# Kernel tuning notes

Measured on AMD Instinct MI355X. Metric: run time of the kernel, lower is better.

## Reference

```python
import jax, jax.numpy as jnp
import numpy as np

N_EMBD = 1024  # C in forward; scale is C**-0.5 (full embed dim, per source)


def setup_inputs() -> dict:
    key = jax.random.key(0)
    k1, k2, k3, k4 = jax.random.split(key, 4)
    B, T, C, H = 4, 4096, N_EMBD, 64
    x = jax.random.normal(k1, (B, T, C), dtype=jnp.float32)
    # weights stored as [in, out] = [n_embd, head_size]
    Wq = jax.random.normal(k2, (C, H), dtype=jnp.float32) * (C ** -0.5)
    Wk = jax.random.normal(k3, (C, H), dtype=jnp.float32) * (C ** -0.5)
    Wv = jax.random.normal(k4, (C, H), dtype=jnp.float32) * (C ** -0.5)
    return {"x": x, "Wq": Wq, "Wk": Wk, "Wv": Wv}


def reference(x, Wq, Wk, Wv):
    # x: [B, T, C]; projections to head_size H
    C = x.shape[-1]
    q = jnp.einsum('btc,ch->bth', x, Wq)  # [B,T,H]
    k = jnp.einsum('btc,ch->bth', x, Wk)  # [B,T,H]
    v = jnp.einsum('btc,ch->bth', x, Wv)  # [B,T,H]
    # scores scaled by C**-0.5 (full embed dim, matching original module)
    wei = jnp.einsum('bth,bsh->bts', q, k) * (C ** -0.5)  # [B,T,T]
    wei = jax.nn.softmax(wei, axis=-1)  # dropout p=0 -> identity
    out = jnp.einsum('bts,bsh->bth', wei, v)  # [B,T,H]
    return out
```

## Files before the change

kernel.cpp:

```cpp
#include <hip/hip_runtime.h>
#include <hip/hip_bf16.h>


#define BB 4
#define TT 4096
#define CC 1024
#define HH 64

typedef __attribute__((ext_vector_type(8))) short bf16x8;
typedef __attribute__((ext_vector_type(4))) float f32x4;

#if __has_builtin(__builtin_amdgcn_exp2f)
#define EXP2(x) __builtin_amdgcn_exp2f(x)
#else
#define EXP2(x) exp2f(x)
#endif

__device__ __forceinline__ short f2bf(float f) {
  union { float f; unsigned u; } v; v.f = f;
  unsigned r = v.u + 0x7fffu + ((v.u >> 16) & 1u);
  return (short)(r >> 16);
}

__device__ __forceinline__ unsigned pk2bf(float lo, float hi) {
  __hip_bfloat162 p = __float22bfloat162_rn(make_float2(lo, hi));
  return *reinterpret_cast<unsigned*>(&p);
}

__global__ void wtf_kernel(const float* __restrict__ Wq, const float* __restrict__ Wk,
                           const float* __restrict__ Wv, short* __restrict__ WtF) {
  int idx = blockIdx.x * 256 + threadIdx.x;
  int lane = idx & 63, ks = (idx >> 6) & 31, nf = idx >> 11;
  int l15 = lane & 15, lg = lane >> 4;
  int n = nf * 16 + l15;
  const float* W = (n < HH) ? Wq : ((n < 2 * HH) ? Wk : Wv);
  float sc = (n < HH) ? (0.03125f * 1.44269504f) : 1.0f;
  int k0 = ks * 32 + lg * 8, h = n & (HH - 1);
  bf16x8 r;
#pragma unroll
  for (int j = 0; j < 8; ++j) r[j] = f2bf(W[(k0 + j) * HH + h] * sc);
  *(bf16x8*)(WtF + (size_t)idx * 8) = r;
}

__launch_bounds__(256, 4)
__global__ void proj_kernel(const float* __restrict__ x, const short* __restrict__ WtF,
                            short* __restrict__ qo, short* __restrict__ kFo,
                            short* __restrict__ vFo) {
  __shared__ __align__(16) short xs[16 * 1024];
  int t = threadIdx.x;
  int row0 = blockIdx.x * 16;

  {
    int r = t >> 4, kc = t & 15;
    const float4* xr4 = (const float4*)(x + (size_t)(row0 + r) * CC) + kc * 2;
#pragma unroll
    for (int i = 0; i < 8; ++i) {
      float4 a = xr4[i * 32], b2 = xr4[i * 32 + 1];
      uint4 w;
      w.x = pk2bf(a.x, a.y);   w.y = pk2bf(a.z, a.w);
      w.z = pk2bf(b2.x, b2.y); w.w = pk2bf(b2.z, b2.w);
      int c = kc + i * 16;
      int S = (c * 256 + r * 16) ^ ((c & 7) << 4);
      *(uint4*)((char*)xs + S) = w;
    }
  }
  __syncthreads();

  int wave = t >> 6, lane = t & 63;
  int l15 = lane & 15, lg = lane >> 4;
  int nf0 = wave * 3;
  const short* wp = WtF + ((size_t)nf0 * 32 * 64 + (size_t)lane) * 8;
  const char* xsb = (const char*)xs;

  f32x4 acc[3];
#pragma unroll
  for (int j = 0; j < 3; ++j) acc[j] = (f32x4){0.f, 0.f, 0.f, 0.f};

  bf16x8 wA[3], wB[3];
#pragma unroll
  for (int j = 0; j < 3; ++j) wA[j] = *(const bf16x8*)(wp + (size_t)j * 32 * 512);

#pragma unroll
  for (int ks = 0; ks < 32; ks += 2) {
#pragma unroll
    for (int j = 0; j < 3; ++j)
      wB[j] = *(const bf16x8*)(wp + ((size_t)j * 32 + ks + 1) * 512);
    bf16x8 a0 = *(const bf16x8*)(xsb + ks * 1024 +
                   ((lane * 16) ^ ((((ks * 4) + lg) & 7) << 4)));
#pragma unroll
    for (int j = 0; j < 3; ++j)
      acc[j] = __builtin_amdgcn_mfma_f32_16x16x32_bf16(a0, wA[j], acc[j], 0, 0, 0);
    if (ks + 2 < 32) {
#pragma unroll
      for (int j = 0; j < 3; ++j)
        wA[j] = *(const bf16x8*)(wp + ((size_t)j * 32 + ks + 2) * 512);
    }
    bf16x8 a1 = *(const bf16x8*)(xsb + (ks + 1) * 1024 +
                   ((lane * 16) ^ (((((ks + 1) * 4) + lg) & 7) << 4)));
#pragma unroll
    for (int j = 0; j < 3; ++j)
      acc[j] = __builtin_amdgcn_mfma_f32_16x16x32_bf16(a1, wB[j], acc[j], 0, 0, 0);
  }

  int b  = row0 >> 12;
  int kt = (row0 & 4095) >> 6;
  int cf = (row0 >> 4) & 3;
  short* ksl = xs;
  short* vsl = xs + 1152;

  __syncthreads();

#pragma unroll
  for (int j = 0; j < 3; ++j) {
    int nf = nf0 + j;
    int h = (nf & 3) * 16 + l15;
    if (nf < 4) {
#pragma unroll
      for (int reg = 0; reg < 4; ++reg)
        qo[(size_t)(row0 + lg * 4 + reg) * HH + h] = f2bf(acc[j][reg]);
    } else if (nf < 8) {
#pragma unroll
      for (int reg = 0; reg < 4; ++reg)
        ksl[(lg * 4 + reg) * 72 + h] = f2bf(acc[j][reg]);
    } else {
      uint2 w2;
      w2.x = pk2bf(acc[j][0], acc[j][1]);
      w2.y = pk2bf(acc[j][2], acc[j][3]);
      *(uint2*)(vsl + h * 24 + lg * 4) = w2;
    }
  }
  __syncthreads();

  size_t tileoff = ((size_t)b * 64 + kt) * 4096;
  if (t < 128) {
    int ks2 = t >> 6, ln = t & 63;
    int l15o = ln & 15, lgo = ln >> 4;
    bf16x8 r = *(const bf16x8*)(ksl + l15o * 72 + ks2 * 32 + lgo * 8);
    *(bf16x8*)(kFo + tileoff + (size_t)(cf * 2 + ks2) * 512 + ln * 8) = r;
  } else if (t < 256) {
    int t2 = t - 128;
    int hf = t2 >> 5, lgl = (t2 >> 4) & 1, l15o = t2 & 15;
    bf16x8 r = *(const bf16x8*)(vsl + (hf * 16 + l15o) * 24 + lgl * 8);
    int lnout = (2 * (cf & 1) + lgl) * 16 + l15o;
    *(bf16x8*)(vFo + tileoff + (size_t)(hf * 2 + (cf >> 1)) * 512 + lnout * 8) = r;
  }
}

__launch_bounds__(512, 4)
__global__ void attnW_kernel(const short* __restrict__ q, const short* __restrict__ kF,
                             const short* __restrict__ vF, float* __restrict__ out) {
  __shared__ __align__(16) short ps[8][2560];
  __shared__ __align__(16) float macc[32][68];
  __shared__ float lL[32];
  int wave = threadIdx.x >> 6, lane = threadIdx.x & 63;
  int l15 = lane & 15, lg = lane >> 4;
  int low3 = blockIdx.x & 7;
  int b  = low3 >> 1;
  int qt = ((blockIdx.x >> 3) << 1) | (low3 & 1);
  int brow0 = qt * 32;

  const short* qb = q + ((size_t)b * TT + brow0 + l15) * HH;
  bf16x8 qa[2][2];
#pragma unroll
  for (int g = 0; g < 2; ++g) {
    qa[g][0] = *(const bf16x8*)(qb + g * 16 * HH + lg * 8);
    qa[g][1] = *(const bf16x8*)(qb + g * 16 * HH + 32 + lg * 8);
  }

  bf16x8 ones;
#pragma unroll
  for (int j = 0; j < 8; ++j) ones[j] = (short)0x3F80;

  const short* kfb = kF + (size_t)b * 262144 + (size_t)lane * 8;
  const short* vfb = vF + (size_t)b * 262144 + (size_t)lane * 8;

  f32x4 acc[2][4], accl[2];
#pragma unroll
  for (int g = 0; g < 2; ++g) {
#pragma unroll
    for (int i = 0; i < 4; ++i) acc[g][i] = (f32x4){0.f, 0.f, 0.f, 0.f};
    accl[g] = (f32x4){0.f, 0.f, 0.f, 0.f};
  }

  char* psw = (char*)&ps[wave][0];
  int xorv = (l15 >> 3) << 4;
  int pwbase = l15 * 80;
  int pr = l15 * 80 + ((lg << 4) ^ xorv);

  for (int t = wave * 16; t < wave * 16 + 16; ++t) {
    const short* kp = kfb + (size_t)t * 2048;
    const short* vp = vfb + (size_t)(t >> 1) * 4096 + (size_t)(t & 1) * 512;
    bf16x8 kf[4], vf[4];
#pragma unroll
    for (int ld = 0; ld < 4; ++ld) kf[ld] = *(const bf16x8*)(kp + ld * 512);
#pragma unroll
    for (int hf = 0; hf < 4; ++hf) vf[hf] = *(const bf16x8*)(vp + hf * 1024);
#pragma unroll
    for (int g = 0; g < 2; ++g)
#pragma unroll
      for (int cf = 0; cf < 2; ++cf) {
        f32x4 t4 = (f32x4){0.f, 0.f, 0.f, 0.f};
        t4 = __builtin_amdgcn_mfma_f32_16x16x32_bf16(kf[cf * 2], qa[g][0], t4, 0, 0, 0);
        t4 = __builtin_amdgcn_mfma_f32_16x16x32_bf16(kf[cf * 2 + 1], qa[g][1], t4, 0, 0, 0);
        float p0 = EXP2(t4[0]), p1 = EXP2(t4[1]);
        float p2 = EXP2(t4[2]), p3 = EXP2(t4[3]);
        unsigned w01 = pk2bf(p0, p1);
        unsigned w23 = pk2bf(p2, p3);
        int cb = (cf << 5) + (lg << 3);
        *(unsigned*)(psw + g * 1280 + pwbase + ((cb) ^ xorv)) = w01;
        *(unsigned*)(psw + g * 1280 + pwbase + ((cb + 4) ^ xorv)) = w23;
      }
    bf16x8 pa0 = *(const bf16x8*)(psw + pr);
    bf16x8 pa1 = *(const bf16x8*)(psw + 1280 + pr);
    __builtin_amdgcn_s_setprio(1);
#pragma unroll
    for (int hf = 0; hf < 4; ++hf) {
      acc[0][hf] = __builtin_amdgcn_mfma_f32_16x16x32_bf16(pa0, vf[hf], acc[0][hf], 0, 0, 0);
      acc[1][hf] = __builtin_amdgcn_mfma_f32_16x16x32_bf16(pa1, vf[hf], acc[1][hf], 0, 0, 0);
    }
    accl[0] = __builtin_amdgcn_mfma_f32_16x16x32_bf16(pa0, ones, accl[0], 0, 0, 0);
    accl[1] = __builtin_amdgcn_mfma_f32_16x16x32_bf16(pa1, ones, accl[1], 0, 0, 0);
    __builtin_amdgcn_s_setprio(0);
  }

#pragma unroll
  for (int ph = 0; ph < 8; ++ph) {
    if (wave == ph) {
#pragma unroll
      for (int g = 0; g < 2; ++g)
#pragma unroll
        for (int reg = 0; reg < 4; ++reg) {
          int row = g * 16 + lg * 4 + reg;
          if (ph == 0) {
#pragma unroll
            for (int hf = 0; hf < 4; ++hf)
              macc[row][hf * 16 + l15] = acc[g][hf][reg];
            if (l15 == 0) lL[row] = accl[g][reg];
          } else {
#pragma unroll
            for (int hf = 0; hf < 4; ++hf)
              macc[row][hf * 16 + l15] += acc[g][hf][reg];
            if (l15 == 0) lL[row] += accl[g][reg];
          }
        }
    }
    __syncthreads();
  }

  {
    int tt = threadIdx.x;
    int r = tt >> 4, c0 = (tt & 15) * 4;
    float linv = 1.0f / lL[r];
    float4 o;
    o.x = macc[r][c0 + 0] * linv; o.y = macc[r][c0 + 1] * linv;
    o.z = macc[r][c0 + 2] * linv; o.w = macc[r][c0 + 3] * linv;
    *(float4*)(out + ((size_t)b * TT + brow0 + r) * HH + c0) = o;
  }
}

extern "C" void kernel_launch(void* const* d_in, const int* in_sizes, int n_in,
                              void* d_out, int out_size, void* d_ws, size_t ws_size,
                              hipStream_t stream) {
  const float* x  = (const float*)d_in[0];
  const float* Wq = (const float*)d_in[1];
  const float* Wk = (const float*)d_in[2];
  const float* Wv = (const float*)d_in[3];
  float* out = (float*)d_out;

  char* ws = (char*)d_ws;
  short* WtF = (short*)ws;
  short* q   = (short*)(ws + 0x080000);
  short* kF  = (short*)(ws + 0x280000);
  short* vF  = (short*)(ws + 0x480000);

  hipLaunchKernelGGL(wtf_kernel,   dim3(96),   dim3(256), 0, stream, Wq, Wk, Wv, WtF);
  hipLaunchKernelGGL(proj_kernel,  dim3(1024), dim3(256), 0, stream, x, WtF, q, kF, vF);
  hipLaunchKernelGGL(attnW_kernel, dim3(512),  dim3(512), 0, stream, q, kF, vF, out);
}
```

Baseline: 64.14 us.

## Pre-convert x to bf16 fragment layout and load it via global_load_lds

Adds a separate kernel that converts x from fp32 to bf16 and writes it in MFMA fragment order into workspace. The projection kernel then copies its tile straight into LDS with global_load_lds instead of converting in registers with swizzled stores, and reads fragments without swizzle math. The aim is to make the projection's load path cheaper and asynchronous. The cost is an extra launch plus a write and re-read of 32 MB of bf16 data, which may cost more than it saves since the projection is memory bound on x.

```diff
diff --git a/kernel.cpp b/kernel.cpp
--- a/kernel.cpp
+++ b/kernel.cpp
@@ -27,6 +27,14 @@
   return *reinterpret_cast<unsigned*>(&p);
 }
 
+__device__ __forceinline__ void gload16(const short* g, short* l) {
+  __builtin_amdgcn_global_load_lds(
+      (const __attribute__((address_space(1))) void*)g,
+      (__attribute__((address_space(3))) void*)l, 16, 0, 0);
+}
+
+#define WAITVM0() asm volatile("s_waitcnt vmcnt(0)" ::: "memory")
+
 __global__ void wtf_kernel(const float* __restrict__ Wq, const float* __restrict__ Wk,
                            const float* __restrict__ Wv, short* __restrict__ WtF) {
   int idx = blockIdx.x * 256 + threadIdx.x;
@@ -42,39 +50,45 @@
   *(bf16x8*)(WtF + (size_t)idx * 8) = r;
 }
 
+__global__ void xc_kernel(const float* __restrict__ x, short* __restrict__ xF) {
+  int idx = blockIdx.x * 256 + threadIdx.x;
+  int lane = idx & 63, ks = (idx >> 6) & 31, rt = idx >> 11;
+  int l15 = lane & 15, lg = lane >> 4;
+  const float4* src = (const float4*)(x + (size_t)(rt * 16 + l15) * CC + ks * 32 + lg * 8);
+  float4 a = src[0], b = src[1];
+  uint4 w;
+  w.x = pk2bf(a.x, a.y);  w.y = pk2bf(a.z, a.w);
+  w.z = pk2bf(b.x, b.y);  w.w = pk2bf(b.z, b.w);
+  *(uint4*)(xF + (size_t)idx * 8) = w;
+}
+
 __launch_bounds__(256, 4)
-__global__ void proj_kernel(const float* __restrict__ x, const short* __restrict__ WtF,
-                            short* __restrict__ qo, short* __restrict__ kFo,
-                            short* __restrict__ vFo) {
-  __shared__ __align__(16) short xs[16 * 1024];
+__global__ void projG_kernel(const short* __restrict__ xF, const short* __restrict__ WtF,
+                             short* __restrict__ qo, short* __restrict__ kFo,
+                             short* __restrict__ vFo) {
+  __shared__ __align__(16) short xs[16384];
   int t = threadIdx.x;
   int row0 = blockIdx.x * 16;
+  int wave = t >> 6, lane = t & 63;
+  int l15 = lane & 15, lg = lane >> 4;
 
   {
-    int r = t >> 4, kc = t & 15;
-    const float4* xr4 = (const float4*)(x + (size_t)(row0 + r) * CC) + kc * 2;
-#pragma unroll
-    for (int i = 0; i < 8; ++i) {
-      float4 a = xr4[i * 32], b2 = xr4[i * 32 + 1];
-      uint4 w;
-      w.x = pk2bf(a.x, a.y);   w.y = pk2bf(a.z, a.w);
-      w.z = pk2bf(b2.x, b2.y); w.w = pk2bf(b2.z, b2.w);
-      int c = kc + i * 16;
-      int S = (c * 256 + r * 16) ^ ((c & 7) << 4);
-      *(uint4*)((char*)xs + S) = w;
-    }
-  }
-  __syncthreads();
-
-  int wave = t >> 6, lane = t & 63;
-  int l15 = lane & 15, lg = lane >> 4;
+    const short* gsrc = xF + (size_t)blockIdx.x * 16384 + ((size_t)wave * 512 + lane) * 8;
+    short* ldst = xs + (size_t)wave * 4096;
+#pragma unroll
+    for (int k2 = 0; k2 < 8; ++k2)
+      gload16(gsrc + k2 * 512, ldst + k2 * 512);
+  }
+
   int nf0 = wave * 3;
   const short* wp = WtF + ((size_t)nf0 * 32 * 64 + (size_t)lane) * 8;
-  const char* xsb = (const char*)xs;
 
   f32x4 acc[3];
 #pragma unroll
   for (int j = 0; j < 3; ++j) acc[j] = (f32x4){0.f, 0.f, 0.f, 0.f};
+
+  WAITVM0();
+  __syncthreads();
 
   bf16x8 wA[3], wB[3];
 #pragma unroll
@@ -85,8 +99,7 @@
 #pragma unroll
     for (int j = 0; j < 3; ++j)
       wB[j] = *(const bf16x8*)(wp + ((size_t)j * 32 + ks + 1) * 512);
-    bf16x8 a0 = *(const bf16x8*)(xsb + ks * 1024 +
-                   ((lane * 16) ^ ((((ks * 4) + lg) & 7) << 4)));
+    bf16x8 a0 = *(const bf16x8*)(xs + ks * 512 + lane * 8);
 #pragma unroll
     for (int j = 0; j < 3; ++j)
       acc[j] = __builtin_amdgcn_mfma_f32_16x16x32_bf16(a0, wA[j], acc[j], 0, 0, 0);
@@ -95,8 +108,7 @@
       for (int j = 0; j < 3; ++j)
         wA[j] = *(const bf16x8*)(wp + ((size_t)j * 32 + ks + 2) * 512);
     }
-    bf16x8 a1 = *(const bf16x8*)(xsb + (ks + 1) * 1024 +
-                   ((lane * 16) ^ (((((ks + 1) * 4) + lg) & 7) << 4)));
+    bf16x8 a1 = *(const bf16x8*)(xs + (ks + 1) * 512 + lane * 8);
 #pragma unroll
     for (int j = 0; j < 3; ++j)
       acc[j] = __builtin_amdgcn_mfma_f32_16x16x32_bf16(a1, wB[j], acc[j], 0, 0, 0);
@@ -272,8 +284,10 @@
   short* q   = (short*)(ws + 0x080000);
   short* kF  = (short*)(ws + 0x280000);
   short* vF  = (short*)(ws + 0x480000);
+  short* xF  = (short*)(ws + 0x680000);
 
   hipLaunchKernelGGL(wtf_kernel,   dim3(96),   dim3(256), 0, stream, Wq, Wk, Wv, WtF);
-  hipLaunchKernelGGL(proj_kernel,  dim3(1024), dim3(256), 0, stream, x, WtF, q, kF, vF);
+  hipLaunchKernelGGL(xc_kernel,    dim3(8192), dim3(256), 0, stream, x, xF);
+  hipLaunchKernelGGL(projG_kernel, dim3(1024), dim3(256), 0, stream, xF, WtF, q, kF, vF);
   hipLaunchKernelGGL(attnW_kernel, dim3(512),  dim3(512), 0, stream, q, kF, vF, out);
 }
```

Measured after the change: 73.82 us. 1.15x slower.

## Stream projection weights into LDS with an async multi-stage global_load_lds ring

Applied to the files above, without the earlier changes.

The projection kernel no longer double-buffers weight fragments in registers. It issues asynchronous global_load_lds transfers into a 4-slot per-wave LDS ring, prefetching three k-steps ahead and gating each step with explicit vmcnt waits. The goal is to hide weight-fetch latency behind the MFMA loop and free registers. The cost is an extra 48KB of LDS per block and launch bounds dropped from 4 to 2, so occupancy for the x-streaming phase falls.

```diff
diff --git a/kernel.cpp b/kernel.cpp
--- a/kernel.cpp
+++ b/kernel.cpp
@@ -26,6 +26,14 @@
   __hip_bfloat162 p = __float22bfloat162_rn(make_float2(lo, hi));
   return *reinterpret_cast<unsigned*>(&p);
 }
+
+__device__ __forceinline__ void gload16(const short* g, short* l) {
+  __builtin_amdgcn_global_load_lds(
+      (const __attribute__((address_space(1))) void*)g,
+      (__attribute__((address_space(3))) void*)l, 16, 0, 0);
+}
+
+#define WAITVM(N) asm volatile("s_waitcnt vmcnt(" #N ")" ::: "memory")
 
 __global__ void wtf_kernel(const float* __restrict__ Wq, const float* __restrict__ Wk,
                            const float* __restrict__ Wv, short* __restrict__ WtF) {
@@ -42,13 +50,16 @@
   *(bf16x8*)(WtF + (size_t)idx * 8) = r;
 }
 
-__launch_bounds__(256, 4)
-__global__ void proj_kernel(const float* __restrict__ x, const short* __restrict__ WtF,
-                            short* __restrict__ qo, short* __restrict__ kFo,
-                            short* __restrict__ vFo) {
-  __shared__ __align__(16) short xs[16 * 1024];
+__launch_bounds__(256, 2)
+__global__ void projP_kernel(const float* __restrict__ x, const short* __restrict__ WtF,
+                             short* __restrict__ qo, short* __restrict__ kFo,
+                             short* __restrict__ vFo) {
+  __shared__ __align__(16) short xs[16384];
+  __shared__ __align__(16) short wlds[24576];
   int t = threadIdx.x;
   int row0 = blockIdx.x * 16;
+  int wave = t >> 6, lane = t & 63;
+  int l15 = lane & 15, lg = lane >> 4;
 
   {
     int r = t >> 4, kc = t & 15;
@@ -66,40 +77,41 @@
   }
   __syncthreads();
 
-  int wave = t >> 6, lane = t & 63;
-  int l15 = lane & 15, lg = lane >> 4;
   int nf0 = wave * 3;
   const short* wp = WtF + ((size_t)nf0 * 32 * 64 + (size_t)lane) * 8;
+  short* wbase = wlds + wave * 1536;
+
+#pragma unroll
+  for (int kp = 0; kp < 3; ++kp)
+#pragma unroll
+    for (int j = 0; j < 3; ++j)
+      gload16(wp + ((size_t)j * 32 + kp) * 512, wbase + kp * 6144 + j * 512);
+
+  f32x4 acc[3];
+#pragma unroll
+  for (int j = 0; j < 3; ++j) acc[j] = (f32x4){0.f, 0.f, 0.f, 0.f};
   const char* xsb = (const char*)xs;
 
-  f32x4 acc[3];
-#pragma unroll
-  for (int j = 0; j < 3; ++j) acc[j] = (f32x4){0.f, 0.f, 0.f, 0.f};
-
-  bf16x8 wA[3], wB[3];
-#pragma unroll
-  for (int j = 0; j < 3; ++j) wA[j] = *(const bf16x8*)(wp + (size_t)j * 32 * 512);
-
-#pragma unroll
-  for (int ks = 0; ks < 32; ks += 2) {
-#pragma unroll
-    for (int j = 0; j < 3; ++j)
-      wB[j] = *(const bf16x8*)(wp + ((size_t)j * 32 + ks + 1) * 512);
-    bf16x8 a0 = *(const bf16x8*)(xsb + ks * 1024 +
-                   ((lane * 16) ^ ((((ks * 4) + lg) & 7) << 4)));
-#pragma unroll
-    for (int j = 0; j < 3; ++j)
-      acc[j] = __builtin_amdgcn_mfma_f32_16x16x32_bf16(a0, wA[j], acc[j], 0, 0, 0);
-    if (ks + 2 < 32) {
+#pragma unroll
+  for (int ks = 0; ks < 32; ++ks) {
+    if (ks <= 29)      { WAITVM(6); }
+    else if (ks == 30) { WAITVM(3); }
+    else               { WAITVM(0); }
+    const short* wb = wbase + (ks % 4) * 6144;
+    bf16x8 w0 = *(const bf16x8*)(wb + 0 * 512 + lane * 8);
+    bf16x8 w1 = *(const bf16x8*)(wb + 1 * 512 + lane * 8);
+    bf16x8 w2 = *(const bf16x8*)(wb + 2 * 512 + lane * 8);
+    bf16x8 a = *(const bf16x8*)(xsb + ks * 1024 +
+                  ((lane * 16) ^ ((((ks * 4) + lg) & 7) << 4)));
+    acc[0] = __builtin_amdgcn_mfma_f32_16x16x32_bf16(a, w0, acc[0], 0, 0, 0);
+    acc[1] = __builtin_amdgcn_mfma_f32_16x16x32_bf16(a, w1, acc[1], 0, 0, 0);
+    acc[2] = __builtin_amdgcn_mfma_f32_16x16x32_bf16(a, w2, acc[2], 0, 0, 0);
+    if (ks + 3 < 32) {
 #pragma unroll
       for (int j = 0; j < 3; ++j)
-        wA[j] = *(const bf16x8*)(wp + ((size_t)j * 32 + ks + 2) * 512);
-    }
-    bf16x8 a1 = *(const bf16x8*)(xsb + (ks + 1) * 1024 +
-                   ((lane * 16) ^ (((((ks + 1) * 4) + lg) & 7) << 4)));
-#pragma unroll
-    for (int j = 0; j < 3; ++j)
-      acc[j] = __builtin_amdgcn_mfma_f32_16x16x32_bf16(a1, wB[j], acc[j], 0, 0, 0);
+        gload16(wp + ((size_t)j * 32 + ks + 3) * 512,
+                wbase + ((ks + 3) % 4) * 6144 + j * 512);
+    }
   }
 
   int b  = row0 >> 12;
@@ -274,6 +286,6 @@
   short* vF  = (short*)(ws + 0x480000);
 
   hipLaunchKernelGGL(wtf_kernel,   dim3(96),   dim3(256), 0, stream, Wq, Wk, Wv, WtF);
-  hipLaunchKernelGGL(proj_kernel,  dim3(1024), dim3(256), 0, stream, x, WtF, q, kF, vF);
+  hipLaunchKernelGGL(projP_kernel, dim3(1024), dim3(256), 0, stream, x, WtF, q, kF, vF);
   hipLaunchKernelGGL(attnW_kernel, dim3(512),  dim3(512), 0, stream, q, kF, vF, out);
 }
```

New measurement: 65.50 us. 1.02x slower.
